# Optimization experiments

Hardware: AMD Instinct MI355X
Metric: run time of the kernel (lower is better)

The kernel has to match this reference:

```python
import jax, jax.numpy as jnp
import numpy as np

EMBED_DIM = 1024
NUM_HEADS = 16
FFN_DIM = 4096
N_QUBITS = 8
LN_EPS = 1e-5


def _layernorm(x, g, b):
    mu = jnp.mean(x, axis=-1, keepdims=True)
    var = jnp.mean(jnp.square(x - mu), axis=-1, keepdims=True)
    return (x - mu) * jax.lax.rsqrt(var + LN_EPS) * g + b


def setup_inputs() -> dict:
    key = jax.random.key(0)
    ks = jax.random.split(key, 12)
    E, F_, Q = EMBED_DIM, FFN_DIM, N_QUBITS
    s = 1.0 / np.sqrt(E)
    return {
        "x": jax.random.normal(ks[0], (4, 2048, E), dtype=jnp.float32),
        "wq": jax.random.normal(ks[1], (E, E), dtype=jnp.float32) * s,
        "wk": jax.random.normal(ks[2], (E, E), dtype=jnp.float32) * s,
        "wv": jax.random.normal(ks[3], (E, E), dtype=jnp.float32) * s,
        "wo": jax.random.normal(ks[4], (E, E), dtype=jnp.float32) * s,
        "theta": jax.random.normal(ks[5], (Q,), dtype=jnp.float32),
        "w1": jax.random.normal(ks[6], (Q, F_), dtype=jnp.float32) * (1.0 / np.sqrt(Q)),
        "w2": jax.random.normal(ks[7], (F_, E), dtype=jnp.float32) * (1.0 / np.sqrt(F_)),
        "ln1_g": jnp.ones((E,), dtype=jnp.float32),
        "ln1_b": jnp.zeros((E,), dtype=jnp.float32),
        "ln2_g": jnp.ones((E,), dtype=jnp.float32),
        "ln2_b": jnp.zeros((E,), dtype=jnp.float32),
    }


def reference(x, wq, wk, wv, wo, theta, w1, w2, ln1_g, ln1_b, ln2_g, ln2_b):
    B, S, E = x.shape
    H, Dk = NUM_HEADS, E // NUM_HEADS
    # ---- multi-head attention ----
    q = (x @ wq).reshape(B, S, H, Dk).transpose(0, 2, 1, 3)  # [B,H,S,Dk]
    k = (x @ wk).reshape(B, S, H, Dk).transpose(0, 2, 1, 3)
    v = (x @ wv).reshape(B, S, H, Dk).transpose(0, 2, 1, 3)
    scores = jnp.einsum("bhsd,bhtd->bhst", q, k) / np.sqrt(Dk)
    attn = jax.nn.softmax(scores, axis=-1)
    ctx = jnp.einsum("bhst,bhtd->bhsd", attn, v)
    ctx = ctx.transpose(0, 2, 1, 3).reshape(B, S, E)
    attn_out = ctx @ wo
    x1 = _layernorm(x + attn_out, ln1_g, ln1_b)
    # ---- quantum FFN ----
    # Per qubit w: |0> -> RX(x1_w) -> RX(x1_w) -> RX(theta_w); <Z> = cos(2*x1_w + theta_w)
    q_out = jnp.cos(2.0 * x1[..., :N_QUBITS] + theta)  # [B,S,Q]
    ffn_out = jax.nn.relu(q_out @ w1) @ w2  # [B,S,E]
    return _layernorm(x1 + ffn_out, ln2_g, ln2_b)
```

## Files before the change

kernel.cpp:

```cpp
#include <hip/hip_runtime.h>
#include <hip/hip_bf16.h>


typedef __attribute__((ext_vector_type(8))) short bf16x8;
typedef __attribute__((ext_vector_type(16))) float f32x16;
typedef __attribute__((ext_vector_type(4))) unsigned short u16x4;

__device__ __forceinline__ unsigned short f2bf(float f) {
  union { float f; unsigned int u; } v; v.f = f;
  return (unsigned short)((v.u + 0x7FFFu + ((v.u >> 16) & 1u)) >> 16);
}
__device__ __forceinline__ float bf2f(unsigned short h) {
  union { unsigned int u; float f; } v; v.u = ((unsigned int)h) << 16;
  return v.f;
}
__device__ __forceinline__ f32x16 mfma32(bf16x8 a, bf16x8 b, f32x16 c) {
  return __builtin_amdgcn_mfma_f32_32x32x16_bf16(a, b, c, 0, 0, 0);
}
__device__ __forceinline__ void lds_cp16(const void* g, void* l) {
  __builtin_amdgcn_global_load_lds(
      (const __attribute__((address_space(1))) unsigned int*)g,
      (__attribute__((address_space(3))) unsigned int*)l, 16, 0, 0);
}

#define QG_CONV(P, FC0, FC1)                                                  \
  {                                                                           \
    int x0a, x0b, x1a, x1b, x2a, x2b, x3a, x3b;                               \
    asm("v_cvt_pk_bf16_f32 %0, %1, %2" : "=v"(x0a) : "v"(P[0]),  "v"(P[1]));  \
    asm("v_cvt_pk_bf16_f32 %0, %1, %2" : "=v"(x0b) : "v"(P[2]),  "v"(P[3]));  \
    asm("v_cvt_pk_bf16_f32 %0, %1, %2" : "=v"(x1a) : "v"(P[4]),  "v"(P[5]));  \
    asm("v_cvt_pk_bf16_f32 %0, %1, %2" : "=v"(x1b) : "v"(P[6]),  "v"(P[7]));  \
    asm("v_cvt_pk_bf16_f32 %0, %1, %2" : "=v"(x2a) : "v"(P[8]),  "v"(P[9]));  \
    asm("v_cvt_pk_bf16_f32 %0, %1, %2" : "=v"(x2b) : "v"(P[10]), "v"(P[11])); \
    asm("v_cvt_pk_bf16_f32 %0, %1, %2" : "=v"(x3a) : "v"(P[12]), "v"(P[13])); \
    asm("v_cvt_pk_bf16_f32 %0, %1, %2" : "=v"(x3b) : "v"(P[14]), "v"(P[15])); \
    asm("v_permlane32_swap_b32 %0, %1" : "+v"(x0a), "+v"(x1a));               \
    asm("v_permlane32_swap_b32 %0, %1" : "+v"(x0b), "+v"(x1b));               \
    asm("v_permlane32_swap_b32 %0, %1" : "+v"(x2a), "+v"(x3a));               \
    asm("v_permlane32_swap_b32 %0, %1" : "+v"(x2b), "+v"(x3b));               \
    union { int u[4]; bf16x8 v; } f0_, f1_;                                   \
    f0_.u[0] = x0a; f0_.u[1] = x0b; f0_.u[2] = x1a; f0_.u[3] = x1b;           \
    f1_.u[0] = x2a; f1_.u[1] = x2b; f1_.u[2] = x3a; f1_.u[3] = x3b;           \
    FC0 = f0_.v; FC1 = f1_.v;                                                 \
  }

__global__ __launch_bounds__(256) void cast_x_kernel(const float* __restrict__ in,
                                                     unsigned short* __restrict__ out,
                                                     int n4) {
  int i = blockIdx.x * 256 + threadIdx.x;
  if (i >= n4) return;
  float4 v = ((const float4*)in)[i];
  u16x4 o = { f2bf(v.x), f2bf(v.y), f2bf(v.z), f2bf(v.w) };
  ((u16x4*)out)[i] = o;
}

__global__ __launch_bounds__(256) void prep_weights(const float* __restrict__ wq,
                                                    const float* __restrict__ wk,
                                                    const float* __restrict__ wv,
                                                    const float* __restrict__ wo,
                                                    const float* __restrict__ w2,
                                                    const float* __restrict__ w1,
                                                    unsigned short* __restrict__ wqkvT,
                                                    unsigned short* __restrict__ woT,
                                                    unsigned short* __restrict__ w2T,
                                                    unsigned short* __restrict__ w1t) {
  __shared__ float tile[32][33];
  const int tx = threadIdx.x, ty = threadIdx.y;
  const int z = blockIdx.z;

  if (z == 0 && blockIdx.y >= 32) {
    if (blockIdx.y < 48) {
      const int f = (blockIdx.y - 32) * 256 + ty * 32 + tx;
      unsigned short v[8];
#pragma unroll
      for (int q = 0; q < 8; q++) v[q] = f2bf(w1[q * 4096 + f]);
      *(u16x4*)(w1t + f * 8)     = (u16x4){v[0], v[1], v[2], v[3]};
      *(u16x4*)(w1t + f * 8 + 4) = (u16x4){v[4], v[5], v[6], v[7]};
    }
    return;
  }
  if (z < 4 && blockIdx.y >= 32) return;

  const float* src;
  unsigned short* dst;
  int K;
  if (z == 4)      { src = w2; dst = w2T; K = 4096; }
  else if (z == 0) { src = wq; dst = wqkvT; K = 1024; }
  else if (z == 1) { src = wk; dst = wqkvT + 1024 * 1024; K = 1024; }
  else if (z == 2) { src = wv; dst = wqkvT + 2048 * 1024; K = 1024; }
  else             { src = wo; dst = woT; K = 1024; }
  const int N = 1024;
  const int n0 = blockIdx.x * 32, k0 = blockIdx.y * 32;
#pragma unroll
  for (int i = 0; i < 32; i += 8)
    tile[ty + i][tx] = src[(long)(k0 + ty + i) * N + n0 + tx];
  __syncthreads();
#pragma unroll
  for (int i = 0; i < 32; i += 8)
    dst[(long)(n0 + ty + i) * K + k0 + tx] = f2bf(tile[tx][ty + i]);
}

__global__ __launch_bounds__(256) void vt_kernel(const unsigned short* __restrict__ qkv,
                                                 unsigned short* __restrict__ vT) {
  __shared__ unsigned short tile[32][34];
  const int t0 = blockIdx.x * 32, d0 = blockIdx.y * 32, bh = blockIdx.z;
  const int b = bh >> 4, h = bh & 15;
  const int tx = threadIdx.x, ty = threadIdx.y;
  const unsigned short* src = qkv + (long)(b * 2048 + t0) * 3072 + 2048 + h * 64 + d0;
#pragma unroll
  for (int i = 0; i < 32; i += 8)
    tile[ty + i][tx] = src[(long)(ty + i) * 3072 + tx];
  __syncthreads();
  unsigned short* dst = vT + ((long)bh * 64 + d0) * 2048 + t0;
#pragma unroll
  for (int i = 0; i < 32; i += 8)
    dst[(long)(ty + i) * 2048 + tx] = tile[tx][ty + i];
}

template<int EPI>
__global__ __launch_bounds__(256) void gemm_bt3(const unsigned short* __restrict__ A,
                                                const unsigned short* __restrict__ BT,
                                                void* __restrict__ Cv,
                                                int M, int N, int K) {
  __shared__ __align__(16) unsigned char smem[2][32768];
  const int tid = threadIdx.x;
  const int l = tid & 63, w = tid >> 6;
  const int l32 = l & 31, h32 = l >> 5;
  const int wrm = (w >> 1) * 64;
  const int wrn = (w & 1) * 64;

  const int nx = gridDim.x;
  const int nwg = nx * gridDim.y;
  const int orig = blockIdx.y * nx + blockIdx.x;
  const int chunk = nwg >> 3;
  const int logical = (orig & 7) * chunk + (orig >> 3);
  const long m0 = (long)(logical / nx) * 128;
  const long n0 = (long)(logical % nx) * 128;

  const unsigned short* gp[8];
  unsigned ldsoff[8];
#pragma unroll
  for (int i = 0; i < 8; i++) {
    const int c = (i & 3) * 256 + tid;
    const int r = c >> 3, k8 = c & 7;
    if (i < 4) {
      gp[i] = A + (m0 + r) * (long)K + (k8 ^ (r & 7)) * 8;
      ldsoff[i] = (unsigned)c * 16;
    } else {
      gp[i] = BT + (n0 + r) * (long)K + (k8 ^ (r & 7)) * 8;
      ldsoff[i] = 16384u + (unsigned)c * 16;
    }
  }

  f32x16 acc[2][2];
#pragma unroll
  for (int mf = 0; mf < 2; mf++)
#pragma unroll
    for (int nf = 0; nf < 2; nf++)
#pragma unroll
      for (int e = 0; e < 16; e++) acc[mf][nf][e] = 0.f;

  const int NT = K >> 6;
#define STAGE(bf, t)                                                    \
  do {                                                                  \
    unsigned char* _d = &smem[bf][0];                                   \
    const long _ko = (long)(t) * 64;                                    \
    _Pragma("unroll")                                                   \
    for (int _i = 0; _i < 8; _i++)                                      \
      lds_cp16(gp[_i] + _ko, _d + ldsoff[_i]);                          \
  } while (0)

  STAGE(0, 0);
  int cur = 0;
  for (int t = 0; t < NT; t++) {
    if (t + 1 < NT) {
      STAGE(cur ^ 1, t + 1);
      asm volatile("s_waitcnt vmcnt(8)" ::: "memory");
    } else {
      asm volatile("s_waitcnt vmcnt(0)" ::: "memory");
    }
    __builtin_amdgcn_sched_barrier(0);
    __builtin_amdgcn_s_barrier();
    __builtin_amdgcn_sched_barrier(0);

    const unsigned char* bufA = &smem[cur][0];
    const unsigned char* bufB = &smem[cur][16384];
    bf16x8 af[2][4], bfr[2][4];
#pragma unroll
    for (int mf = 0; mf < 2; mf++) {
      const int r = wrm + mf * 32 + l32;
#pragma unroll
      for (int ks = 0; ks < 4; ks++)
        af[mf][ks] = *(const bf16x8*)(bufA + r * 128 + (((ks * 2 + h32) ^ (r & 7)) * 16));
    }
#pragma unroll
    for (int nf = 0; nf < 2; nf++) {
      const int r = wrn + nf * 32 + l32;
#pragma unroll
      for (int ks = 0; ks < 4; ks++)
        bfr[nf][ks] = *(const bf16x8*)(bufB + r * 128 + (((ks * 2 + h32) ^ (r & 7)) * 16));
    }
    __builtin_amdgcn_s_setprio(1);
#pragma unroll
    for (int ks = 0; ks < 4; ks++)
#pragma unroll
      for (int mf = 0; mf < 2; mf++)
#pragma unroll
        for (int nf = 0; nf < 2; nf++)
          acc[mf][nf] = mfma32(af[mf][ks], bfr[nf][ks], acc[mf][nf]);
    __builtin_amdgcn_s_setprio(0);
    __builtin_amdgcn_sched_barrier(0);
    __builtin_amdgcn_s_barrier();
    cur ^= 1;
  }
#undef STAGE

#pragma unroll
  for (int mf = 0; mf < 2; mf++)
#pragma unroll
    for (int nf = 0; nf < 2; nf++) {
      const long c0 = n0 + wrn + nf * 32 + l32;
#pragma unroll
      for (int reg = 0; reg < 16; reg++) {
        const long r0 = m0 + wrm + mf * 32 + (reg & 3) + 8 * (reg >> 2) + 4 * h32;
        if (EPI == 0) ((float*)Cv)[r0 * (long)N + c0] = acc[mf][nf][reg];
        else ((unsigned short*)Cv)[r0 * (long)N + c0] = f2bf(acc[mf][nf][reg]);
      }
    }
}

__global__ __launch_bounds__(512) void ffn_fused(const unsigned short* __restrict__ qo,
                                                 const unsigned short* __restrict__ w1t,
                                                 const unsigned short* __restrict__ BT,
                                                 unsigned short* __restrict__ Cp0,
                                                 unsigned short* __restrict__ Cp1,
                                                 int N, int K) {
  __shared__ __align__(16) unsigned char sm[2 * 16384 + 32768 + 4096];
  unsigned char* lsW = sm + 32768;
  unsigned char* lsQ = sm + 65536;
  const int tid = threadIdx.x;
  const int l = tid & 63, w = tid >> 6;
  const int l32 = l & 31, h32 = l >> 5;
  const int wrm = (w >> 1) * 64;
  const int wrn = (w & 1) * 64;

  const int nx = gridDim.x;
  const int nwg = nx * gridDim.y;
  const int orig = blockIdx.y * nx + blockIdx.x;
  const int chunk = nwg >> 3;
  const int logical = (orig & 7) * chunk + (orig >> 3);
  const long m0 = (long)(logical / nx) * 256;
  const long n0 = (long)(logical % nx) * 128;
  const int kz = blockIdx.z;
  const int NT = (K >> 6) >> 1;
  const int tbase = kz * NT;
  unsigned short* C = kz ? Cp1 : Cp0;

  const unsigned short* gpB[2];
  unsigned offB[2];
#pragma unroll
  for (int i = 0; i < 2; i++) {
    const int c = i * 512 + tid;
    const int r = c >> 3, k8 = c & 7;
    gpB[i] = BT + (n0 + r) * (long)K + (long)tbase * 64 + (k8 ^ (r & 7)) * 8;
    offB[i] = (unsigned)c * 16;
  }
  const unsigned short* w1base = w1t + (long)tbase * 64 * 8;

  const bf16x8 z8 = {0, 0, 0, 0, 0, 0, 0, 0};

#define STAGE_B(bf, t)                                                  \
  do {                                                                  \
    unsigned char* _d = sm + (bf) * 16384;                              \
    const long _ko = (long)(t) * 64;                                    \
    lds_cp16(gpB[0] + _ko, _d + offB[0]);                               \
    lds_cp16(gpB[1] + _ko, _d + offB[1]);                               \
  } while (0)

#pragma unroll
  for (int i = 0; i < 4; i++) {
    const int slot = i * 8 + w;
    lds_cp16(w1base + (long)(slot * 64 + l) * 8, lsW + ((unsigned)slot << 10));
  }
  if (w < 4) lds_cp16(qo + (m0 + w * 64 + l) * 8, lsQ + (unsigned)(w * 64) * 16);
  STAGE_B(0, 0);
  asm volatile("s_waitcnt vmcnt(0)" ::: "memory");
  __builtin_amdgcn_s_barrier();

  bf16x8 qof[2];
#pragma unroll
  for (int mf = 0; mf < 2; mf++)
    qof[mf] = (h32 == 0) ? *(const bf16x8*)(lsQ + (wrm + mf * 32 + l32) * 16) : z8;

  f32x16 zz;
#pragma unroll
  for (int e = 0; e < 16; e++) zz[e] = 0.f;
  f32x16 acc[2][2];
#pragma unroll
  for (int mf = 0; mf < 2; mf++)
#pragma unroll
    for (int nf = 0; nf < 2; nf++) acc[mf][nf] = zz;

  f32x16 hP0, hP1;
  {
    bf16x8 wf0 = (h32 == 0) ? *(const bf16x8*)(lsW + (0 + l32) * 16) : z8;
    bf16x8 wf1 = (h32 == 0) ? *(const bf16x8*)(lsW + (32 + l32) * 16) : z8;
    hP0 = mfma32(wf0, qof[0], zz);
    hP1 = mfma32(wf1, qof[0], zz);
  }

  int cur = 0;
  for (int t = 0; t < NT; t++) {
    if (t + 1 < NT) {
      STAGE_B(cur ^ 1, t + 1);
      asm volatile("s_waitcnt vmcnt(2)" ::: "memory");
    } else {
      asm volatile("s_waitcnt vmcnt(0)" ::: "memory");
    }
    __builtin_amdgcn_sched_barrier(0);
    __builtin_amdgcn_s_barrier();
    __builtin_amdgcn_sched_barrier(0);

    bf16x8 w1ft[2], w1fn[2];
#pragma unroll
    for (int tg = 0; tg < 2; tg++) {
      w1ft[tg] = (h32 == 0)
          ? *(const bf16x8*)(lsW + ((unsigned)t << 10) + (tg * 32 + l32) * 16) : z8;
      w1fn[tg] = (h32 == 0 && t + 1 < NT)
          ? *(const bf16x8*)(lsW + ((unsigned)(t + 1) << 10) + (tg * 32 + l32) * 16) : z8;
    }
    const unsigned char* bufB = sm + cur * 16384;
    bf16x8 bfr[2][4];
#pragma unroll
    for (int nf = 0; nf < 2; nf++) {
      const int r = wrn + nf * 32 + l32;
#pragma unroll
      for (int ks = 0; ks < 4; ks++)
        bfr[nf][ks] = *(const bf16x8*)(bufB + r * 128 + (((ks * 2 + h32) ^ (r & 7)) * 16));
    }

#pragma unroll
    for (int e = 0; e < 16; e++) {
      hP0[e] = fmaxf(hP0[e], 0.f);
      hP1[e] = fmaxf(hP1[e], 0.f);
    }
    bf16x8 a0, a1, a2, a3;
    QG_CONV(hP0, a0, a1)
    QG_CONV(hP1, a2, a3)
    __builtin_amdgcn_s_setprio(1);
    f32x16 hQ0 = mfma32(w1ft[0], qof[1], zz);
    f32x16 hQ1 = mfma32(w1ft[1], qof[1], zz);
    acc[0][0] = mfma32(a0, bfr[0][0], acc[0][0]);
    acc[0][0] = mfma32(a1, bfr[0][1], acc[0][0]);
    acc[0][0] = mfma32(a2, bfr[0][2], acc[0][0]);
    acc[0][0] = mfma32(a3, bfr[0][3], acc[0][0]);
    acc[0][1] = mfma32(a0, bfr[1][0], acc[0][1]);
    acc[0][1] = mfma32(a1, bfr[1][1], acc[0][1]);
    acc[0][1] = mfma32(a2, bfr[1][2], acc[0][1]);
    acc[0][1] = mfma32(a3, bfr[1][3], acc[0][1]);
    __builtin_amdgcn_s_setprio(0);

#pragma unroll
    for (int e = 0; e < 16; e++) {
      hQ0[e] = fmaxf(hQ0[e], 0.f);
      hQ1[e] = fmaxf(hQ1[e], 0.f);
    }
    bf16x8 b0, b1, b2, b3;
    QG_CONV(hQ0, b0, b1)
    QG_CONV(hQ1, b2, b3)
    __builtin_amdgcn_s_setprio(1);
    hP0 = mfma32(w1fn[0], qof[0], zz);
    hP1 = mfma32(w1fn[1], qof[0], zz);
    acc[1][0] = mfma32(b0, bfr[0][0], acc[1][0]);
    acc[1][0] = mfma32(b1, bfr[0][1], acc[1][0]);
    acc[1][0] = mfma32(b2, bfr[0][2], acc[1][0]);
    acc[1][0] = mfma32(b3, bfr[0][3], acc[1][0]);
    acc[1][1] = mfma32(b0, bfr[1][0], acc[1][1]);
    acc[1][1] = mfma32(b1, bfr[1][1], acc[1][1]);
    acc[1][1] = mfma32(b2, bfr[1][2], acc[1][1]);
    acc[1][1] = mfma32(b3, bfr[1][3], acc[1][1]);
    __builtin_amdgcn_s_setprio(0);

    __builtin_amdgcn_sched_barrier(0);
    __builtin_amdgcn_s_barrier();
    cur ^= 1;
  }
#undef STAGE_B

#pragma unroll
  for (int mf = 0; mf < 2; mf++)
#pragma unroll
    for (int nf = 0; nf < 2; nf++) {
      const long c0 = n0 + wrn + nf * 32 + l32;
#pragma unroll
      for (int reg = 0; reg < 16; reg++) {
        const long r0 = m0 + wrm + mf * 32 + (reg & 3) + 8 * (reg >> 2) + 4 * h32;
        C[r0 * (long)N + c0] = f2bf(acc[mf][nf][reg]);
      }
    }
}

#define QG_BLOCK(P, LIP, FC0, FC1)                                            \
  {                                                                           \
    _Pragma("unroll")                                                         \
    for (int e = 0; e < 16; e++)                                              \
      asm("v_exp_f32 %0, %1" : "=v"(P[e]) : "v"(P[e]));                       \
    float s_ = 0.f;                                                           \
    _Pragma("unroll")                                                         \
    for (int e = 0; e < 16; e++) s_ += P[e];                                  \
    LIP += s_;                                                                \
    QG_CONV(P, FC0, FC1)                                                      \
  }

__global__ __launch_bounds__(256) void attn_kernel(const unsigned short* __restrict__ qkv,
                                                   const unsigned short* __restrict__ vT,
                                                   unsigned short* __restrict__ ctx) {
  __shared__ __align__(16) unsigned short lsK[64][72];
  __shared__ __align__(16) unsigned short lsV[64][72];

  const int tid = threadIdx.x;
  const int l = tid & 63, w = tid >> 6;
  const int l32 = l & 31, h32 = l >> 5;

  const int orig = blockIdx.x;
  const int logical = (orig & 7) * 64 + (orig >> 3);
  const int s0 = (logical & 7) * 256;
  const int bh = logical >> 3;
  const int b = bh >> 4, hh = bh & 15;

  const float QSC = 0.18033688f;
  const unsigned short* qg_base = qkv + (long)(b * 2048 + s0 + w * 64) * 3072 + hh * 64;
  bf16x8 qb0[4], qb1[4];
#pragma unroll
  for (int kc = 0; kc < 4; kc++) {
    bf16x8 t0v = *(const bf16x8*)(qg_base + (long)l32 * 3072 + kc * 16 + h32 * 8);
    bf16x8 t1v = *(const bf16x8*)(qg_base + (long)(32 + l32) * 3072 + kc * 16 + h32 * 8);
#pragma unroll
    for (int j = 0; j < 8; j++) {
      t0v[j] = (short)f2bf(bf2f((unsigned short)t0v[j]) * QSC);
      t1v[j] = (short)f2bf(bf2f((unsigned short)t1v[j]) * QSC);
    }
    qb0[kc] = t0v;
    qb1[kc] = t1v;
  }

  f32x16 oacc00, oacc01, oacc10, oacc11;
#pragma unroll
  for (int e = 0; e < 16; e++) {
    oacc00[e] = 0.f; oacc01[e] = 0.f; oacc10[e] = 0.f; oacc11[e] = 0.f;
  }
  float lip0 = 0.f, lip1 = 0.f;

  const int tr = tid >> 2;
  const int tc = (tid & 3) * 16;
  const unsigned short* kbase = qkv + (long)(b * 2048) * 3072 + 1024 + hh * 64;
  const unsigned short* vbase = vT + (long)bh * 64 * 2048;

  bf16x8 k0 = *(const bf16x8*)(kbase + (long)tr * 3072 + tc);
  bf16x8 k1 = *(const bf16x8*)(kbase + (long)tr * 3072 + tc + 8);
  bf16x8 v0 = *(const bf16x8*)(vbase + (long)tr * 2048 + tc);
  bf16x8 v1 = *(const bf16x8*)(vbase + (long)tr * 2048 + tc + 8);

  for (int t0 = 0; t0 < 2048; t0 += 64) {
    __syncthreads();
    *(bf16x8*)&lsK[tr][tc]     = k0;
    *(bf16x8*)&lsK[tr][tc + 8] = k1;
    *(bf16x8*)&lsV[tr][tc]     = v0;
    *(bf16x8*)&lsV[tr][tc + 8] = v1;
    __syncthreads();
    if (t0 + 64 < 2048) {
      k0 = *(const bf16x8*)(kbase + (long)(t0 + 64 + tr) * 3072 + tc);
      k1 = *(const bf16x8*)(kbase + (long)(t0 + 64 + tr) * 3072 + tc + 8);
      v0 = *(const bf16x8*)(vbase + (long)tr * 2048 + t0 + 64 + tc);
      v1 = *(const bf16x8*)(vbase + (long)tr * 2048 + t0 + 64 + tc + 8);
    }

#pragma unroll
    for (int tg = 0; tg < 2; tg++) {
      bf16x8 kb[4];
#pragma unroll
      for (int kc = 0; kc < 4; kc++)
        kb[kc] = *(const bf16x8*)&lsK[tg * 32 + l32][kc * 16 + h32 * 8];

      f32x16 p0, p1;
#pragma unroll
      for (int e = 0; e < 16; e++) { p0[e] = 0.f; p1[e] = 0.f; }
      __builtin_amdgcn_s_setprio(1);
#pragma unroll
      for (int kc = 0; kc < 4; kc++) {
        p0 = mfma32(kb[kc], qb0[kc], p0);
        p1 = mfma32(kb[kc], qb1[kc], p1);
      }
      __builtin_amdgcn_s_setprio(0);

      bf16x8 fA0, fA1, fB0, fB1;
      QG_BLOCK(p0, lip0, fA0, fA1)
      QG_BLOCK(p1, lip1, fB0, fB1)

      bf16x8 v00 = *(const bf16x8*)&lsV[l32][tg * 32 + h32 * 8];
      bf16x8 v01 = *(const bf16x8*)&lsV[l32][tg * 32 + 16 + h32 * 8];
      bf16x8 v10 = *(const bf16x8*)&lsV[32 + l32][tg * 32 + h32 * 8];
      bf16x8 v11 = *(const bf16x8*)&lsV[32 + l32][tg * 32 + 16 + h32 * 8];

      __builtin_amdgcn_s_setprio(1);
      oacc00 = mfma32(fA0, v00, oacc00);
      oacc00 = mfma32(fA1, v01, oacc00);
      oacc01 = mfma32(fA0, v10, oacc01);
      oacc01 = mfma32(fA1, v11, oacc01);
      oacc10 = mfma32(fB0, v00, oacc10);
      oacc10 = mfma32(fB1, v01, oacc10);
      oacc11 = mfma32(fB0, v10, oacc11);
      oacc11 = mfma32(fB1, v11, oacc11);
      __builtin_amdgcn_s_setprio(0);
    }
  }

  const float li0 = lip0 + __shfl_xor(lip0, 32);
  const float li1 = lip1 + __shfl_xor(lip1, 32);
  const float inv0 = 1.f / li0;
  const float inv1 = 1.f / li1;
  const long qrow0 = (long)(b * 2048 + s0 + w * 64);
  const int dcol = hh * 64 + l32;
#define STORE_QG(OA, OB, INV, QOFF)                                           \
  _Pragma("unroll")                                                           \
  for (int reg = 0; reg < 16; reg++) {                                        \
    const int rq = (reg & 3) + 8 * (reg >> 2) + 4 * h32;                      \
    const float iv = __shfl(INV, rq);                                         \
    const long q = qrow0 + (QOFF) + rq;                                       \
    ctx[q * 1024 + dcol]      = f2bf(OA[reg] * iv);                           \
    ctx[q * 1024 + dcol + 32] = f2bf(OB[reg] * iv);                           \
  }
  STORE_QG(oacc00, oacc01, inv0, 0)
  STORE_QG(oacc10, oacc11, inv1, 32)
#undef STORE_QG
}

__global__ __launch_bounds__(256) void ln1_kernel(const float* __restrict__ x,
                                                  const unsigned short* __restrict__ ao,
                                                  const float* __restrict__ g,
                                                  const float* __restrict__ bb,
                                                  unsigned short* __restrict__ x1,
                                                  unsigned short* __restrict__ qo,
                                                  const float* __restrict__ theta) {
  const int row = blockIdx.x;
  const int tid = threadIdx.x;
  const long base = (long)row * 1024 + tid * 4;
  float4 a = *(const float4*)(x + base);
  u16x4 o = *(const u16x4*)(ao + base);
  float4 r;
  r.x = a.x + bf2f(o[0]); r.y = a.y + bf2f(o[1]);
  r.z = a.z + bf2f(o[2]); r.w = a.w + bf2f(o[3]);
  float s  = r.x + r.y + r.z + r.w;
  float ss = r.x * r.x + r.y * r.y + r.z * r.z + r.w * r.w;
  for (int off = 32; off; off >>= 1) {
    s  += __shfl_down(s, off);
    ss += __shfl_down(ss, off);
  }
  __shared__ float red[4][2];
  const int wv = tid >> 6;
  if ((tid & 63) == 0) { red[wv][0] = s; red[wv][1] = ss; }
  __syncthreads();
  s  = red[0][0] + red[1][0] + red[2][0] + red[3][0];
  ss = red[0][1] + red[1][1] + red[2][1] + red[3][1];
  const float mu  = s * (1.f / 1024.f);
  const float var = ss * (1.f / 1024.f) - mu * mu;
  const float rsv = rsqrtf(var + 1e-5f);
  float4 gv  = *(const float4*)(g + tid * 4);
  float4 bbv = *(const float4*)(bb + tid * 4);
  float y0 = (r.x - mu) * rsv * gv.x + bbv.x;
  float y1 = (r.y - mu) * rsv * gv.y + bbv.y;
  float y2 = (r.z - mu) * rsv * gv.z + bbv.z;
  float y3 = (r.w - mu) * rsv * gv.w + bbv.w;
  *(u16x4*)(x1 + base) = (u16x4){f2bf(y0), f2bf(y1), f2bf(y2), f2bf(y3)};
  if (tid < 2) {
    float yv[4] = {y0, y1, y2, y3};
    u16x4 q;
#pragma unroll
    for (int c = 0; c < 4; c++)
      q[c] = f2bf(__cosf(2.f * yv[c] + theta[tid * 4 + c]));
    *(u16x4*)(qo + (long)row * 8 + tid * 4) = q;
  }
}

__global__ __launch_bounds__(256) void ln2_kernel(const unsigned short* __restrict__ x1,
                                                  const unsigned short* __restrict__ p0,
                                                  const unsigned short* __restrict__ p1,
                                                  const float* __restrict__ g,
                                                  const float* __restrict__ bb,
                                                  float* __restrict__ out) {
  const int row = blockIdx.x;
  const int tid = threadIdx.x;
  const long base = (long)row * 1024 + tid * 4;
  u16x4 a = *(const u16x4*)(x1 + base);
  u16x4 b = *(const u16x4*)(p0 + base);
  u16x4 c = *(const u16x4*)(p1 + base);
  float4 r;
  r.x = bf2f(a[0]) + bf2f(b[0]) + bf2f(c[0]);
  r.y = bf2f(a[1]) + bf2f(b[1]) + bf2f(c[1]);
  r.z = bf2f(a[2]) + bf2f(b[2]) + bf2f(c[2]);
  r.w = bf2f(a[3]) + bf2f(b[3]) + bf2f(c[3]);
  float s  = r.x + r.y + r.z + r.w;
  float ss = r.x * r.x + r.y * r.y + r.z * r.z + r.w * r.w;
  for (int off = 32; off; off >>= 1) {
    s  += __shfl_down(s, off);
    ss += __shfl_down(ss, off);
  }
  __shared__ float red[4][2];
  const int wv = tid >> 6;
  if ((tid & 63) == 0) { red[wv][0] = s; red[wv][1] = ss; }
  __syncthreads();
  s  = red[0][0] + red[1][0] + red[2][0] + red[3][0];
  ss = red[0][1] + red[1][1] + red[2][1] + red[3][1];
  const float mu  = s * (1.f / 1024.f);
  const float var = ss * (1.f / 1024.f) - mu * mu;
  const float rsv = rsqrtf(var + 1e-5f);
  float4 gv  = *(const float4*)(g + tid * 4);
  float4 bbv = *(const float4*)(bb + tid * 4);
  float4 y;
  y.x = (r.x - mu) * rsv * gv.x + bbv.x;
  y.y = (r.y - mu) * rsv * gv.y + bbv.y;
  y.z = (r.z - mu) * rsv * gv.z + bbv.z;
  y.w = (r.w - mu) * rsv * gv.w + bbv.w;
  *(float4*)(out + base) = y;
}

extern "C" void kernel_launch(void* const* d_in, const int* in_sizes, int n_in,
                              void* d_out, int out_size, void* d_ws, size_t ws_size,
                              hipStream_t stream) {
  const float* x     = (const float*)d_in[0];
  const float* wq    = (const float*)d_in[1];
  const float* wk    = (const float*)d_in[2];
  const float* wv    = (const float*)d_in[3];
  const float* wo    = (const float*)d_in[4];
  const float* theta = (const float*)d_in[5];
  const float* w1    = (const float*)d_in[6];
  const float* w2    = (const float*)d_in[7];
  const float* g1    = (const float*)d_in[8];
  const float* b1    = (const float*)d_in[9];
  const float* g2    = (const float*)d_in[10];
  const float* b2    = (const float*)d_in[11];
  float* out = (float*)d_out;
  char* ws = (char*)d_ws;

  const long MB = 1 << 20;
  unsigned short* xb    = (unsigned short*)(ws);
  unsigned short* wqkvT = (unsigned short*)(ws + 16 * MB);
  unsigned short* woT   = (unsigned short*)(ws + 22 * MB);
  unsigned short* w2T   = (unsigned short*)(ws + 24 * MB);
  unsigned short* x1b   = (unsigned short*)(ws + 32 * MB);
  unsigned short* aob   = (unsigned short*)(ws + 64 * MB);
  unsigned short* p0b   = aob;
  unsigned short* p1b   = (unsigned short*)(ws + 80 * MB);
  unsigned short* qkv   = (unsigned short*)(ws + 96 * MB);
  unsigned short* vTb   = (unsigned short*)(ws + 144 * MB);
  unsigned short* qob   = (unsigned short*)(ws + 160 * MB);
  unsigned short* w1tb  = (unsigned short*)(ws + 160 * MB + 128 * 1024);
  unsigned short* ctx   = xb;

  cast_x_kernel<<<8192, 256, 0, stream>>>(x, xb, 8192 * 1024 / 4);
  dim3 tb(32, 8);
  prep_weights<<<dim3(32, 128, 5), tb, 0, stream>>>(wq, wk, wv, wo, w2, w1,
                                                    wqkvT, woT, w2T, w1tb);

  gemm_bt3<1><<<dim3(24, 64), 256, 0, stream>>>(xb, wqkvT, qkv, 8192, 3072, 1024);

  vt_kernel<<<dim3(64, 2, 64), tb, 0, stream>>>(qkv, vTb);

  attn_kernel<<<512, 256, 0, stream>>>(qkv, vTb, ctx);

  gemm_bt3<1><<<dim3(8, 64), 256, 0, stream>>>(ctx, woT, aob, 8192, 1024, 1024);

  ln1_kernel<<<8192, 256, 0, stream>>>(x, aob, g1, b1, x1b, qob, theta);

  ffn_fused<<<dim3(8, 32, 2), 512, 0, stream>>>(qob, w1tb, w2T, p0b, p1b, 1024, 4096);

  ln2_kernel<<<8192, 256, 0, stream>>>(x1b, p0b, p1b, g2, b2, out);
}
```

Before: 313.1 us.

## Widen fused FFN tile to 256 columns to reuse recomputed hidden activations

The fused FFN kernel now covers 256 output columns per workgroup instead of 128, staging two B sub-tiles per k-step and halving the grid's x dimension. Each workgroup recomputes the hidden activations relu(q·w1) once per k-step and reuses them across twice as many output columns, so the total recompute and the redundant w1/q loads are halved. The software pipelining that overlapped the next step's hidden MFMA with the current accumulation is dropped for a simpler in-step order. In exchange, LDS use roughly doubles, the accumulator register count doubles, and there are only half as many workgroups, which may reduce occupancy.

```diff
diff --git a/kernel.cpp b/kernel.cpp
--- a/kernel.cpp
+++ b/kernel.cpp
@@ -235,9 +235,9 @@
                                                  unsigned short* __restrict__ Cp0,
                                                  unsigned short* __restrict__ Cp1,
                                                  int N, int K) {
-  __shared__ __align__(16) unsigned char sm[2 * 16384 + 32768 + 4096];
-  unsigned char* lsW = sm + 32768;
-  unsigned char* lsQ = sm + 65536;
+  __shared__ __align__(16) unsigned char sm[4 * 16384 + 32768 + 4096];
+  unsigned char* lsW = sm + 65536;
+  unsigned char* lsQ = sm + 98304;
   const int tid = threadIdx.x;
   const int l = tid & 63, w = tid >> 6;
   const int l32 = l & 31, h32 = l >> 5;
@@ -250,19 +250,21 @@
   const int chunk = nwg >> 3;
   const int logical = (orig & 7) * chunk + (orig >> 3);
   const long m0 = (long)(logical / nx) * 256;
-  const long n0 = (long)(logical % nx) * 128;
+  const long n0 = (long)(logical % nx) * 256;
   const int kz = blockIdx.z;
   const int NT = (K >> 6) >> 1;
   const int tbase = kz * NT;
   unsigned short* C = kz ? Cp1 : Cp0;
 
-  const unsigned short* gpB[2];
+  const unsigned short* gpB[2][2];
   unsigned offB[2];
 #pragma unroll
   for (int i = 0; i < 2; i++) {
     const int c = i * 512 + tid;
     const int r = c >> 3, k8 = c & 7;
-    gpB[i] = BT + (n0 + r) * (long)K + (long)tbase * 64 + (k8 ^ (r & 7)) * 8;
+#pragma unroll
+    for (int nt2 = 0; nt2 < 2; nt2++)
+      gpB[nt2][i] = BT + (n0 + nt2 * 128 + r) * (long)K + (long)tbase * 64 + (k8 ^ (r & 7)) * 8;
     offB[i] = (unsigned)c * 16;
   }
   const unsigned short* w1base = w1t + (long)tbase * 64 * 8;
@@ -271,10 +273,13 @@
 
 #define STAGE_B(bf, t)                                                  \
   do {                                                                  \
-    unsigned char* _d = sm + (bf) * 16384;                              \
     const long _ko = (long)(t) * 64;                                    \
-    lds_cp16(gpB[0] + _ko, _d + offB[0]);                               \
-    lds_cp16(gpB[1] + _ko, _d + offB[1]);                               \
+    _Pragma("unroll")                                                   \
+    for (int _n = 0; _n < 2; _n++) {                                    \
+      unsigned char* _d = sm + ((bf) * 2 + _n) * 16384;                 \
+      lds_cp16(gpB[_n][0] + _ko, _d + offB[0]);                         \
+      lds_cp16(gpB[_n][1] + _ko, _d + offB[1]);                         \
+    }                                                                   \
   } while (0)
 
 #pragma unroll
@@ -295,25 +300,19 @@
   f32x16 zz;
 #pragma unroll
   for (int e = 0; e < 16; e++) zz[e] = 0.f;
-  f32x16 acc[2][2];
-#pragma unroll
-  for (int mf = 0; mf < 2; mf++)
-#pragma unroll
-    for (int nf = 0; nf < 2; nf++) acc[mf][nf] = zz;
-
-  f32x16 hP0, hP1;
-  {
-    bf16x8 wf0 = (h32 == 0) ? *(const bf16x8*)(lsW + (0 + l32) * 16) : z8;
-    bf16x8 wf1 = (h32 == 0) ? *(const bf16x8*)(lsW + (32 + l32) * 16) : z8;
-    hP0 = mfma32(wf0, qof[0], zz);
-    hP1 = mfma32(wf1, qof[0], zz);
-  }
+  f32x16 acc[2][2][2];
+#pragma unroll
+  for (int nt2 = 0; nt2 < 2; nt2++)
+#pragma unroll
+    for (int mf = 0; mf < 2; mf++)
+#pragma unroll
+      for (int nf = 0; nf < 2; nf++) acc[nt2][mf][nf] = zz;
 
   int cur = 0;
   for (int t = 0; t < NT; t++) {
     if (t + 1 < NT) {
       STAGE_B(cur ^ 1, t + 1);
-      asm volatile("s_waitcnt vmcnt(2)" ::: "memory");
+      asm volatile("s_waitcnt vmcnt(4)" ::: "memory");
     } else {
       asm volatile("s_waitcnt vmcnt(0)" ::: "memory");
     }
@@ -321,65 +320,61 @@
     __builtin_amdgcn_s_barrier();
     __builtin_amdgcn_sched_barrier(0);
 
-    bf16x8 w1ft[2], w1fn[2];
-#pragma unroll
-    for (int tg = 0; tg < 2; tg++) {
-      w1ft[tg] = (h32 == 0)
+    bf16x8 w1f[2];
+#pragma unroll
+    for (int tg = 0; tg < 2; tg++)
+      w1f[tg] = (h32 == 0)
           ? *(const bf16x8*)(lsW + ((unsigned)t << 10) + (tg * 32 + l32) * 16) : z8;
-      w1fn[tg] = (h32 == 0 && t + 1 < NT)
-          ? *(const bf16x8*)(lsW + ((unsigned)(t + 1) << 10) + (tg * 32 + l32) * 16) : z8;
-    }
-    const unsigned char* bufB = sm + cur * 16384;
-    bf16x8 bfr[2][4];
-#pragma unroll
-    for (int nf = 0; nf < 2; nf++) {
-      const int r = wrn + nf * 32 + l32;
-#pragma unroll
-      for (int ks = 0; ks < 4; ks++)
-        bfr[nf][ks] = *(const bf16x8*)(bufB + r * 128 + (((ks * 2 + h32) ^ (r & 7)) * 16));
-    }
-
+
+    __builtin_amdgcn_s_setprio(1);
+    f32x16 hC0 = mfma32(w1f[0], qof[0], zz);
+    f32x16 hC1 = mfma32(w1f[1], qof[0], zz);
+    f32x16 hD0 = mfma32(w1f[0], qof[1], zz);
+    f32x16 hD1 = mfma32(w1f[1], qof[1], zz);
+    __builtin_amdgcn_s_setprio(0);
 #pragma unroll
     for (int e = 0; e < 16; e++) {
-      hP0[e] = fmaxf(hP0[e], 0.f);
-      hP1[e] = fmaxf(hP1[e], 0.f);
-    }
-    bf16x8 a0, a1, a2, a3;
-    QG_CONV(hP0, a0, a1)
-    QG_CONV(hP1, a2, a3)
-    __builtin_amdgcn_s_setprio(1);
-    f32x16 hQ0 = mfma32(w1ft[0], qof[1], zz);
-    f32x16 hQ1 = mfma32(w1ft[1], qof[1], zz);
-    acc[0][0] = mfma32(a0, bfr[0][0], acc[0][0]);
-    acc[0][0] = mfma32(a1, bfr[0][1], acc[0][0]);
-    acc[0][0] = mfma32(a2, bfr[0][2], acc[0][0]);
-    acc[0][0] = mfma32(a3, bfr[0][3], acc[0][0]);
-    acc[0][1] = mfma32(a0, bfr[1][0], acc[0][1]);
-    acc[0][1] = mfma32(a1, bfr[1][1], acc[0][1]);
-    acc[0][1] = mfma32(a2, bfr[1][2], acc[0][1]);
-    acc[0][1] = mfma32(a3, bfr[1][3], acc[0][1]);
-    __builtin_amdgcn_s_setprio(0);
-
-#pragma unroll
-    for (int e = 0; e < 16; e++) {
-      hQ0[e] = fmaxf(hQ0[e], 0.f);
-      hQ1[e] = fmaxf(hQ1[e], 0.f);
-    }
-    bf16x8 b0, b1, b2, b3;
-    QG_CONV(hQ0, b0, b1)
-    QG_CONV(hQ1, b2, b3)
-    __builtin_amdgcn_s_setprio(1);
-    hP0 = mfma32(w1fn[0], qof[0], zz);
-    hP1 = mfma32(w1fn[1], qof[0], zz);
-    acc[1][0] = mfma32(b0, bfr[0][0], acc[1][0]);
-    acc[1][0] = mfma32(b1, bfr[0][1], acc[1][0]);
-    acc[1][0] = mfma32(b2, bfr[0][2], acc[1][0]);
-    acc[1][0] = mfma32(b3, bfr[0][3], acc[1][0]);
-    acc[1][1] = mfma32(b0, bfr[1][0], acc[1][1]);
-    acc[1][1] = mfma32(b1, bfr[1][1], acc[1][1]);
-    acc[1][1] = mfma32(b2, bfr[1][2], acc[1][1]);
-    acc[1][1] = mfma32(b3, bfr[1][3], acc[1][1]);
-    __builtin_amdgcn_s_setprio(0);
+      hC0[e] = fmaxf(hC0[e], 0.f);
+      hC1[e] = fmaxf(hC1[e], 0.f);
+      hD0[e] = fmaxf(hD0[e], 0.f);
+      hD1[e] = fmaxf(hD1[e], 0.f);
+    }
+    bf16x8 a0, a1, a2, a3, b0, b1, b2, b3;
+    QG_CONV(hC0, a0, a1)
+    QG_CONV(hC1, a2, a3)
+    QG_CONV(hD0, b0, b1)
+    QG_CONV(hD1, b2, b3)
+
+#pragma unroll
+    for (int nt2 = 0; nt2 < 2; nt2++) {
+      const unsigned char* bufB = sm + (cur * 2 + nt2) * 16384;
+      bf16x8 bfr[2][4];
+#pragma unroll
+      for (int nf = 0; nf < 2; nf++) {
+        const int r = wrn + nf * 32 + l32;
+#pragma unroll
+        for (int ks = 0; ks < 4; ks++)
+          bfr[nf][ks] = *(const bf16x8*)(bufB + r * 128 + (((ks * 2 + h32) ^ (r & 7)) * 16));
+      }
+      __builtin_amdgcn_s_setprio(1);
+      acc[nt2][0][0] = mfma32(a0, bfr[0][0], acc[nt2][0][0]);
+      acc[nt2][0][0] = mfma32(a1, bfr[0][1], acc[nt2][0][0]);
+      acc[nt2][0][0] = mfma32(a2, bfr[0][2], acc[nt2][0][0]);
+      acc[nt2][0][0] = mfma32(a3, bfr[0][3], acc[nt2][0][0]);
+      acc[nt2][0][1] = mfma32(a0, bfr[1][0], acc[nt2][0][1]);
+      acc[nt2][0][1] = mfma32(a1, bfr[1][1], acc[nt2][0][1]);
+      acc[nt2][0][1] = mfma32(a2, bfr[1][2], acc[nt2][0][1]);
+      acc[nt2][0][1] = mfma32(a3, bfr[1][3], acc[nt2][0][1]);
+      acc[nt2][1][0] = mfma32(b0, bfr[0][0], acc[nt2][1][0]);
+      acc[nt2][1][0] = mfma32(b1, bfr[0][1], acc[nt2][1][0]);
+      acc[nt2][1][0] = mfma32(b2, bfr[0][2], acc[nt2][1][0]);
+      acc[nt2][1][0] = mfma32(b3, bfr[0][3], acc[nt2][1][0]);
+      acc[nt2][1][1] = mfma32(b0, bfr[1][0], acc[nt2][1][1]);
+      acc[nt2][1][1] = mfma32(b1, bfr[1][1], acc[nt2][1][1]);
+      acc[nt2][1][1] = mfma32(b2, bfr[1][2], acc[nt2][1][1]);
+      acc[nt2][1][1] = mfma32(b3, bfr[1][3], acc[nt2][1][1]);
+      __builtin_amdgcn_s_setprio(0);
+    }
 
     __builtin_amdgcn_sched_barrier(0);
     __builtin_amdgcn_s_barrier();
@@ -388,16 +383,18 @@
 #undef STAGE_B
 
 #pragma unroll
-  for (int mf = 0; mf < 2; mf++)
-#pragma unroll
-    for (int nf = 0; nf < 2; nf++) {
-      const long c0 = n0 + wrn + nf * 32 + l32;
-#pragma unroll
-      for (int reg = 0; reg < 16; reg++) {
-        const long r0 = m0 + wrm + mf * 32 + (reg & 3) + 8 * (reg >> 2) + 4 * h32;
-        C[r0 * (long)N + c0] = f2bf(acc[mf][nf][reg]);
+  for (int nt2 = 0; nt2 < 2; nt2++)
+#pragma unroll
+    for (int mf = 0; mf < 2; mf++)
+#pragma unroll
+      for (int nf = 0; nf < 2; nf++) {
+        const long c0 = n0 + nt2 * 128 + wrn + nf * 32 + l32;
+#pragma unroll
+        for (int reg = 0; reg < 16; reg++) {
+          const long r0 = m0 + wrm + mf * 32 + (reg & 3) + 8 * (reg >> 2) + 4 * h32;
+          C[r0 * (long)N + c0] = f2bf(acc[nt2][mf][nf][reg]);
+        }
       }
-    }
 }
 
 #define QG_BLOCK(P, LIP, FC0, FC1)                                            \
@@ -672,7 +669,7 @@
 
   ln1_kernel<<<8192, 256, 0, stream>>>(x, aob, g1, b1, x1b, qob, theta);
 
-  ffn_fused<<<dim3(8, 32, 2), 512, 0, stream>>>(qob, w1tb, w2T, p0b, p1b, 1024, 4096);
+  ffn_fused<<<dim3(4, 32, 2), 512, 0, stream>>>(qob, w1tb, w2T, p0b, p1b, 1024, 4096);
 
   ln2_kernel<<<8192, 256, 0, stream>>>(x1b, p0b, p1b, g2, b2, out);
 }
```

Measured after the change: 293.5 us (median of 2 runs). 1.07x faster.
